# Kernel tuning notes

Hardware: AMD Instinct MI355X
Metric: run time of the kernel (lower is better)

The kernel has to match this reference:

```python
import jax, jax.numpy as jnp
import numpy as np

B, NX, NY = 4, 128, 128
DIM, DH, HEADS, LATENT, DOUT = 128, 64, 8, 64, 128
KM = 3
KD = DH * KM          # per-head low-rank-kernel dim (192)
SCALING = 1.0         # kernel_multiplier<=4 and softmax=False -> scaling_factor
ROT_SCALE = 64.0      # 1/min_freq of continuous RotaryEmbedding (min_freq=1/64)
EPS = 1e-5


def layer_norm(x, g, b):
    m = x.mean(-1, keepdims=True)
    v = jnp.var(x, axis=-1, keepdims=True)
    return (x - m) * jax.lax.rsqrt(v + EPS) * g + b


def pooling_reducer(x, Win, g, b, W1, b1, W2, b2):
    # x: [b, n, m, c] -> mean over axis 2 -> PreNorm(MLP with gated GELU) -> [b, n, latent]
    h = (x @ Win).mean(axis=2)
    h = layer_norm(h, g, b)
    h = h @ W1 + b1
    c = h.shape[-1] // 2
    h = jax.nn.gelu(h[..., :c], approximate=False) * h[..., c:]
    return h @ W2 + b2


def rotary(t, pos):
    # t: [b,h,n,d], pos: [n] continuous coordinates
    d = t.shape[-1]
    inv_freq = 1.0 / (10000.0 ** (jnp.arange(0, d, 2, dtype=jnp.float32) / d))
    f = (pos * ROT_SCALE)[:, None] * inv_freq          # [n, d//2]
    f = jnp.concatenate([f, f], axis=-1)               # [n, d]
    cos, sin = jnp.cos(f), jnp.sin(f)
    x1, x2 = jnp.split(t, 2, axis=-1)
    rot = jnp.concatenate([-x2, x1], axis=-1)          # rotate_half (half-split variant)
    return t * cos + rot * sin


def low_rank_kernel(u, pos, Wqk):
    # u: [b, n, latent] -> kernel K: [b, h, n, n]
    b, n, _ = u.shape
    qk = u @ Wqk                                       # [b, n, 2*h*KD]
    q, k = jnp.split(qk, 2, axis=-1)
    q = q.reshape(b, n, HEADS, KD).transpose(0, 2, 1, 3)
    k = k.reshape(b, n, HEADS, KD).transpose(0, 2, 1, 3)
    q = rotary(q, pos)
    k = rotary(k, pos)
    return jnp.einsum('bhid,bhjd->bhij', q, k) * SCALING


def setup_inputs():
    key = jax.random.key(0)
    ks = jax.random.split(key, 16)
    s = 0.02
    def rn(k, shape):
        return jax.random.normal(k, shape, dtype=jnp.float32) * s
    return {
        'u': jax.random.normal(ks[0], (B, NX, NY, DIM), dtype=jnp.float32),
        'pos_x': jnp.sort(jax.random.uniform(ks[1], (NX,), dtype=jnp.float32)),
        'pos_y': jnp.sort(jax.random.uniform(ks[2], (NY,), dtype=jnp.float32)),
        'ln_g': jnp.ones((DIM,), jnp.float32),
        'ln_b': jnp.zeros((DIM,), jnp.float32),
        'Wv': rn(ks[3], (DIM, HEADS * DH)),
        'Win': rn(ks[4], (DIM, DIM)),
        'px_Win': rn(ks[5], (DIM, DIM)),
        'px_g': jnp.ones((DIM,), jnp.float32),
        'px_b': jnp.zeros((DIM,), jnp.float32),
        'px_W1': rn(ks[6], (DIM, 2 * DIM)),
        'px_b1': jnp.zeros((2 * DIM,), jnp.float32),
        'px_W2': rn(ks[7], (DIM, LATENT)),
        'px_b2': jnp.zeros((LATENT,), jnp.float32),
        'py_Win': rn(ks[8], (DIM, DIM)),
        'py_g': jnp.ones((DIM,), jnp.float32),
        'py_b': jnp.zeros((DIM,), jnp.float32),
        'py_W1': rn(ks[9], (DIM, 2 * DIM)),
        'py_b1': jnp.zeros((2 * DIM,), jnp.float32),
        'py_W2': rn(ks[10], (DIM, LATENT)),
        'py_b2': jnp.zeros((LATENT,), jnp.float32),
        'Wqk_x': rn(ks[11], (LATENT, 2 * HEADS * KD)),
        'Wqk_y': rn(ks[12], (LATENT, 2 * HEADS * KD)),
        'Wo1': rn(ks[13], (HEADS * DH, DOUT)),
        'Wo2': rn(ks[14], (DOUT, DOUT)),
    }


def reference(u, pos_x, pos_y, ln_g, ln_b, Wv, Win,
              px_Win, px_g, px_b, px_W1, px_b1, px_W2, px_b2,
              py_Win, py_g, py_b, py_W1, py_b1, py_W2, py_b2,
              Wqk_x, Wqk_y, Wo1, Wo2):
    un = layer_norm(u, ln_g, ln_b)                      # [b,nx,ny,dim]
    v = un @ Wv                                         # [b,nx,ny,h*dh]
    ui = un @ Win
    ux = pooling_reducer(ui, px_Win, px_g, px_b, px_W1, px_b1, px_W2, px_b2)                       # [b,nx,L]
    uy = pooling_reducer(ui.transpose(0, 2, 1, 3), py_Win, py_g, py_b, py_W1, py_b1, py_W2, py_b2)  # [b,ny,L]
    kx = low_rank_kernel(ux, pos_x, Wqk_x)              # [b,h,nx,nx]
    ky = low_rank_kernel(uy, pos_y, Wqk_y)              # [b,h,ny,ny]
    b, nx, ny, _ = u.shape
    vphi = v.reshape(b, nx, ny, HEADS, DH).transpose(0, 3, 1, 2, 4)   # b h i l c
    t = jnp.einsum('bhij,bhjmc->bhimc', kx, vphi)       # attend along x axis
    t = jnp.einsum('bhlm,bhimc->bhilc', ky, t)          # attend along y axis
    t = t.transpose(0, 2, 3, 1, 4).reshape(b, nx, ny, HEADS * DH)
    # InstanceNorm2d applied to a channels-LAST tensor (as in the original repo):
    # torch treats dim1 (nx) as channels, normalizing over (ny, h*dh) per (b, nx), no affine.
    m = t.mean(axis=(2, 3), keepdims=True)
    var = t.var(axis=(2, 3), keepdims=True)
    t = (t - m) * jax.lax.rsqrt(var + EPS)
    h = jax.nn.gelu(t @ Wo1, approximate=False)
    return h @ Wo2
```

## Files before the change

kernel.cpp:

```cpp
#include <hip/hip_runtime.h>
#include <math.h>

#define ROWS 65536
#define KDD 192

typedef __attribute__((ext_vector_type(8))) short bfrag;
typedef __attribute__((ext_vector_type(4))) float facc;

__device__ inline unsigned short bf16r(float x) {
  union { float f; unsigned u; } v; v.f = x;
  unsigned r = v.u + 0x7fffu + ((v.u >> 16) & 1u);
  return (unsigned short)(r >> 16);
}
__device__ inline float bf2f(unsigned short h) {
  union { unsigned u; float f; } v; v.u = ((unsigned)h) << 16; return v.f;
}
__device__ inline float gelu_f(float x) {
  return x * 0.5f * (1.f + erff(x * 0.70710678f));
}
__device__ __forceinline__ void gload16(const void* g, void* l) {
  __builtin_amdgcn_global_load_lds((const __attribute__((address_space(1))) unsigned int*)g,
                                   (__attribute__((address_space(3))) unsigned int*)l,
                                   16, 0, 0);
}

__global__ __launch_bounds__(128) void k_ln(const float* __restrict__ x,
                                            const float* __restrict__ g,
                                            const float* __restrict__ bb,
                                            unsigned short* __restrict__ y) {
  int row = blockIdx.x;
  int t = threadIdx.x;
  float v = x[(size_t)row * 128 + t];
  float s = v, s2 = v * v;
  for (int off = 32; off > 0; off >>= 1) {
    s += __shfl_down(s, off, 64);
    s2 += __shfl_down(s2, off, 64);
  }
  __shared__ float ps[2], ps2[2];
  int wid = t >> 6, lane = t & 63;
  if (lane == 0) { ps[wid] = s; ps2[wid] = s2; }
  __syncthreads();
  float S = ps[0] + ps[1], S2 = ps2[0] + ps2[1];
  float mean = S * (1.f / 128.f);
  float var = S2 * (1.f / 128.f) - mean * mean;
  float r = rsqrtf(var + 1e-5f);
  y[(size_t)row * 128 + t] = bf16r((v - mean) * r * g[t] + bb[t]);
}

__global__ __launch_bounds__(128) void k_means(const unsigned short* __restrict__ un,
                                               float* __restrict__ mx, float* __restrict__ my) {
  int blk = blockIdx.x;
  int c = threadIdx.x;
  if (blk < 512) {
    const unsigned short* p = un + (size_t)blk * 16384 + c;
    float s = 0;
    for (int j = 0; j < 128; j++) s += bf2f(p[(size_t)j * 128]);
    mx[(size_t)blk * 128 + c] = s * (1.f / 128.f);
  } else {
    int bj = blk - 512;
    int b = bj >> 7, j = bj & 127;
    const unsigned short* p = un + (size_t)b * 2097152 + (size_t)j * 128 + c;
    float s = 0;
    for (int i = 0; i < 128; i++) s += bf2f(p[(size_t)i * 16384]);
    my[(size_t)bj * 128 + c] = s * (1.f / 128.f);
  }
}

__global__ __launch_bounds__(256) void k_wprep(const float* __restrict__ Wv,
                                               const float* __restrict__ Wo1,
                                               const float* __restrict__ Wo2,
                                               unsigned short* __restrict__ WvT,
                                               unsigned short* __restrict__ Wo1T,
                                               unsigned short* __restrict__ Wo2T,
                                               float* __restrict__ scol) {
  int blk = blockIdx.x, t = threadIdx.x;
  if (blk < 256) {
    int idx = blk * 256 + t;
    int c = idx >> 7, r = idx & 127;
    WvT[(size_t)c * 128 + r] = bf16r(Wv[(size_t)r * 512 + c]);
  } else if (blk < 512) {
    int idx = (blk - 256) * 256 + t;
    int n = idx >> 9, k = idx & 511;
    Wo1T[(size_t)n * 512 + k] = bf16r(Wo1[(size_t)k * 128 + n]);
  } else if (blk < 576) {
    int idx = (blk - 512) * 256 + t;
    int n = idx >> 7, k = idx & 127;
    Wo2T[n * 128 + k] = bf16r(Wo2[k * 128 + n]);
  } else {
    if (t < 128) {
      float a = 0;
      for (int k = 0; k < 512; k++) a += bf2f(bf16r(Wo1[k * 128 + t]));
      scol[t] = a;
    }
  }
}

__global__ __launch_bounds__(256) void k_gemmz(const float* __restrict__ A0,
                                               const float* __restrict__ B0,
                                               float* __restrict__ C0,
                                               const float* __restrict__ A1,
                                               const float* __restrict__ B1,
                                               float* __restrict__ C1,
                                               int K, int lda, int ldb, int ldc) {
  const float* A = blockIdx.z ? A1 : A0;
  const float* Bm = blockIdx.z ? B1 : B0;
  float* C = blockIdx.z ? C1 : C0;
  __shared__ float As[16][64];
  __shared__ float Bs[16][64];
  int tid = threadIdx.x;
  int n0 = blockIdx.x * 64, m0 = blockIdx.y * 64;
  int tx = tid & 15, ty = tid >> 4;
  float acc[4][4] = {};
  int la_m = tid >> 2, la_k = (tid & 3) * 4;
  int lb_k = tid >> 4, lb_n = (tid & 15) * 4;
  for (int k0 = 0; k0 < K; k0 += 16) {
    float4 a4 = *(const float4*)(A + (size_t)(m0 + la_m) * lda + k0 + la_k);
    As[la_k + 0][la_m] = a4.x; As[la_k + 1][la_m] = a4.y;
    As[la_k + 2][la_m] = a4.z; As[la_k + 3][la_m] = a4.w;
    float4 b4 = *(const float4*)(Bm + (size_t)(k0 + lb_k) * ldb + n0 + lb_n);
    *(float4*)&Bs[lb_k][lb_n] = b4;
    __syncthreads();
#pragma unroll
    for (int kk = 0; kk < 16; kk++) {
      float4 av = *(const float4*)&As[kk][ty * 4];
      float4 bv = *(const float4*)&Bs[kk][tx * 4];
      float a[4] = {av.x, av.y, av.z, av.w};
      float b[4] = {bv.x, bv.y, bv.z, bv.w};
#pragma unroll
      for (int i = 0; i < 4; i++)
#pragma unroll
        for (int j = 0; j < 4; j++) acc[i][j] += a[i] * b[j];
    }
    __syncthreads();
  }
#pragma unroll
  for (int i = 0; i < 4; i++) {
    float4 o;
    o.x = acc[i][0]; o.y = acc[i][1]; o.z = acc[i][2]; o.w = acc[i][3];
    *(float4*)(C + (size_t)(m0 + ty * 4 + i) * ldc + n0 + tx * 4) = o;
  }
}

__global__ __launch_bounds__(128) void k_pool2(const float* __restrict__ in0, const float* __restrict__ in1,
                                               const float* __restrict__ Wc0, const float* __restrict__ Wc1,
                                               const float* __restrict__ g0, const float* __restrict__ g1,
                                               const float* __restrict__ bb0, const float* __restrict__ bb1,
                                               const float* __restrict__ W10, const float* __restrict__ W11,
                                               const float* __restrict__ b10, const float* __restrict__ b11,
                                               const float* __restrict__ W20, const float* __restrict__ W21,
                                               const float* __restrict__ b20, const float* __restrict__ b21,
                                               float* __restrict__ o0, float* __restrict__ o1) {
  int sel = blockIdx.y;
  const float* in = sel ? in1 : in0;  const float* Wc = sel ? Wc1 : Wc0;
  const float* g = sel ? g1 : g0;     const float* bb = sel ? bb1 : bb0;
  const float* W1 = sel ? W11 : W10;  const float* b1 = sel ? b11 : b10;
  const float* W2 = sel ? W21 : W20;  const float* b2 = sel ? b21 : b20;
  float* out = sel ? o1 : o0;
  int row = blockIdx.x;
  int t = threadIdx.x;
  __shared__ float xin[128], h1[128], h3[128];
  __shared__ float ps[2], ps2[2];
  xin[t] = in[(size_t)row * 128 + t];
  __syncthreads();
  float a = 0;
  for (int k = 0; k < 128; k++) a += xin[k] * Wc[k * 128 + t];
  float s = a, s2 = a * a;
  for (int off = 32; off > 0; off >>= 1) {
    s += __shfl_down(s, off, 64);
    s2 += __shfl_down(s2, off, 64);
  }
  if ((t & 63) == 0) { ps[t >> 6] = s; ps2[t >> 6] = s2; }
  __syncthreads();
  float S = ps[0] + ps[1], S2 = ps2[0] + ps2[1];
  float mean = S * (1.f / 128.f);
  float var = S2 * (1.f / 128.f) - mean * mean;
  float r = rsqrtf(var + 1e-5f);
  h1[t] = (a - mean) * r * g[t] + bb[t];
  __syncthreads();
  float u1 = b1[t], u2 = b1[t + 128];
  for (int k = 0; k < 128; k++) {
    float hv = h1[k];
    u1 += hv * W1[k * 256 + t];
    u2 += hv * W1[k * 256 + t + 128];
  }
  h3[t] = gelu_f(u1) * u2;
  __syncthreads();
  if (t < 64) {
    float o = b2[t];
    for (int k = 0; k < 128; k++) o += h3[k] * W2[k * 64 + t];
    out[(size_t)row * 64 + t] = o;
  }
}

__global__ __launch_bounds__(192) void k_rot2(const float* __restrict__ qk0, const float* __restrict__ qk1,
                                              const float* __restrict__ pos0, const float* __restrict__ pos1,
                                              float* __restrict__ qr0, float* __restrict__ qr1,
                                              float* __restrict__ kr0, float* __restrict__ kr1) {
  int sel = blockIdx.y;
  const float* qk = sel ? qk1 : qk0;
  const float* pos = sel ? pos1 : pos0;
  float* qr = sel ? qr1 : qr0;
  float* kr = sel ? kr1 : kr0;
  int bn = blockIdx.x;
  int b = bn >> 7, n = bn & 127;
  int d = threadIdx.x;
  int fi = d % 96;
  float inv = expf(-logf(10000.f) * ((float)fi / 96.f));
  float f = pos[n] * 64.f * inv;
  float cs = cosf(f), sn = sinf(f);
  int partner = d < 96 ? d + 96 : d - 96;
  float sgn = d < 96 ? -1.f : 1.f;
  for (int h = 0; h < 8; h++) {
    float q = qk[(size_t)bn * 3072 + h * 192 + d];
    float qp = qk[(size_t)bn * 3072 + h * 192 + partner];
    float kx = qk[(size_t)bn * 3072 + 1536 + h * 192 + d];
    float kp = qk[(size_t)bn * 3072 + 1536 + h * 192 + partner];
    size_t o = ((size_t)(b * 8 + h) * 128 + n) * 192 + d;
    qr[o] = q * cs + sgn * qp * sn;
    kr[o] = kx * cs + sgn * kp * sn;
  }
}

__global__ __launch_bounds__(256) void k_qkt2(const float* __restrict__ Q0, const float* __restrict__ K0,
                                              unsigned short* __restrict__ C0,
                                              const float* __restrict__ Q1, const float* __restrict__ K1,
                                              unsigned short* __restrict__ C1) {
  int z = blockIdx.z;
  int bh = z & 31;
  const float* Qb = (z < 32 ? Q0 : Q1) + (size_t)bh * 128 * KDD;
  const float* Kb = (z < 32 ? K0 : K1) + (size_t)bh * 128 * KDD;
  unsigned short* Cb = (z < 32 ? C0 : C1) + (size_t)bh * 128 * 128;
  __shared__ float As[16][64];
  __shared__ float Bs[16][64];
  int tid = threadIdx.x;
  int i0 = blockIdx.y * 64, j0 = blockIdx.x * 64;
  int tx = tid & 15, ty = tid >> 4;
  float acc[4][4] = {};
  int l_m = tid >> 2, l_k = (tid & 3) * 4;
  for (int k0 = 0; k0 < KDD; k0 += 16) {
    float4 a4 = *(const float4*)(Qb + (size_t)(i0 + l_m) * KDD + k0 + l_k);
    As[l_k + 0][l_m] = a4.x; As[l_k + 1][l_m] = a4.y;
    As[l_k + 2][l_m] = a4.z; As[l_k + 3][l_m] = a4.w;
    float4 b4 = *(const float4*)(Kb + (size_t)(j0 + l_m) * KDD + k0 + l_k);
    Bs[l_k + 0][l_m] = b4.x; Bs[l_k + 1][l_m] = b4.y;
    Bs[l_k + 2][l_m] = b4.z; Bs[l_k + 3][l_m] = b4.w;
    __syncthreads();
#pragma unroll
    for (int kk = 0; kk < 16; kk++) {
      float4 av = *(const float4*)&As[kk][ty * 4];
      float4 bv = *(const float4*)&Bs[kk][tx * 4];
      float a[4] = {av.x, av.y, av.z, av.w};
      float b[4] = {bv.x, bv.y, bv.z, bv.w};
#pragma unroll
      for (int i = 0; i < 4; i++)
#pragma unroll
        for (int j = 0; j < 4; j++) acc[i][j] += a[i] * b[j];
    }
    __syncthreads();
  }
#pragma unroll
  for (int i = 0; i < 4; i++) {
    unsigned h0 = bf16r(acc[i][0]), h1 = bf16r(acc[i][1]);
    unsigned h2 = bf16r(acc[i][2]), h3 = bf16r(acc[i][3]);
    uint2 pk;
    pk.x = h0 | (h1 << 16);
    pk.y = h2 | (h3 << 16);
    *(uint2*)(Cb + (size_t)(i0 + ty * 4 + i) * 128 + j0 + tx * 4) = pk;
  }
}


__global__ __launch_bounds__(256) void k_vt(const unsigned short* __restrict__ WvT,
                                            const unsigned short* __restrict__ un,
                                            unsigned short* __restrict__ vT) {
  int nt = blockIdx.x;
  int mt = blockIdx.y;
  __shared__ __align__(16) unsigned short As[16384];
  __shared__ __align__(16) unsigned short Bs[16384];
  int tid = threadIdx.x;
  int w = tid >> 6, lane = tid & 63, quad = lane >> 4, l16 = lane & 15;
  {
    int r = tid >> 1, half = tid & 1;
    const unsigned short* sa = WvT + (size_t)(mt * 128 + r) * 128 + half * 64;
    const unsigned short* sbp = un + (size_t)(nt * 128 + r) * 128 + half * 64;
#pragma unroll
    for (int q = 0; q < 8; q++) {
      int c8 = half * 8 + q;
      int ph = ((c8 ^ (r & 15)) << 3);
      *(uint4*)&As[r * 128 + ph] = *(const uint4*)(sa + q * 8);
      *(uint4*)&Bs[r * 128 + ph] = *(const uint4*)(sbp + q * 8);
    }
  }
  __syncthreads();
  facc zf = {0.f, 0.f, 0.f, 0.f};
  facc acc[2][8];
#pragma unroll
  for (int a = 0; a < 2; a++)
#pragma unroll
    for (int bq = 0; bq < 8; bq++) acc[a][bq] = zf;
#pragma unroll
  for (int k0 = 0; k0 < 4; k0++) {
    bfrag av[2];
#pragma unroll
    for (int it = 0; it < 2; it++) {
      int row = (w + it * 4) * 16 + l16;
      av[it] = *(const bfrag*)&As[row * 128 + ((((k0 * 4 + quad) ^ l16)) << 3)];
    }
#pragma unroll
    for (int nt8 = 0; nt8 < 8; nt8++) {
      int row = nt8 * 16 + l16;
      bfrag bv = *(const bfrag*)&Bs[row * 128 + ((((k0 * 4 + quad) ^ l16)) << 3)];
      acc[0][nt8] = __builtin_amdgcn_mfma_f32_16x16x32_bf16(av[0], bv, acc[0][nt8], 0, 0, 0);
      acc[1][nt8] = __builtin_amdgcn_mfma_f32_16x16x32_bf16(av[1], bv, acc[1][nt8], 0, 0, 0);
    }
  }
  __syncthreads();
#pragma unroll
  for (int it = 0; it < 2; it++)
#pragma unroll
    for (int nt8 = 0; nt8 < 8; nt8++)
#pragma unroll
      for (int rr = 0; rr < 4; rr++) {
        int row = (w + it * 4) * 16 + quad * 4 + rr;
        int col = nt8 * 16 + l16;
        As[row * 128 + ((((col >> 3) ^ (row & 15)) << 3)) + (col & 7)] = bf16r(acc[it][nt8][rr]);
      }
  __syncthreads();
  {
    int r = tid >> 1, half = tid & 1;
    unsigned short* dst = vT + (size_t)(mt * 128 + r) * 65536 + (size_t)nt * 128 + half * 64;
#pragma unroll
    for (int q = 0; q < 8; q++) {
      int c8 = half * 8 + q;
      *(uint4*)(dst + q * 8) = *(const uint4*)&As[r * 128 + ((c8 ^ (r & 15)) << 3)];
    }
  }
}

__global__ __launch_bounds__(256, 2) void k_fuse12(const unsigned short* __restrict__ kxall,
                                                   const unsigned short* __restrict__ kyall,
                                                   const unsigned short* __restrict__ vT,
                                                   unsigned short* __restrict__ ttp,
                                                   float* __restrict__ sb,
                                                   float* __restrict__ s2b) {
  int blk = blockIdx.x;
  int bh = blk >> 4, strip = blk & 15;
  int b = bh >> 3, h = bh & 7;
  __shared__ __align__(16) unsigned short Ky[16384];
  __shared__ __align__(16) unsigned short Vs[16384];
  int tid = threadIdx.x;
  int w = tid >> 6, lane = tid & 63, quad = lane >> 4, l16 = lane & 15;
  int wr = w >> 1, wc = w & 1;

  {
    const unsigned short* kb = kyall + (size_t)bh * 16384;
#pragma unroll
    for (int q = 0; q < 8; q++) {
      int rbase = w * 32 + q * 4;
      int r = rbase + quad;
      gload16(kb + (size_t)r * 128 + ((l16 ^ (r & 15)) << 3), &Ky[rbase * 128]);
    }
  }
  bfrag axf[4][4];
  {
    const unsigned short* xb = kxall + (size_t)bh * 16384;
#pragma unroll
    for (int it = 0; it < 4; it++) {
      int i = (wr * 4 + it) * 16 + l16;
#pragma unroll
      for (int k0 = 0; k0 < 4; k0++)
        axf[it][k0] = *(const bfrag*)(xb + (size_t)i * 128 + k0 * 32 + quad * 8);
    }
  }

  float s[4] = {0.f, 0.f, 0.f, 0.f}, s2[4] = {0.f, 0.f, 0.f, 0.f};
  facc zf = {0.f, 0.f, 0.f, 0.f};

  for (int cc = 0; cc < 4; cc++) {
    int c = strip * 4 + cc;
    if (cc) __syncthreads();
    {
      const unsigned short* vb = vT + (size_t)(h * 64 + c) * 65536 + (size_t)b * 16384;
#pragma unroll
      for (int q = 0; q < 8; q++) {
        int rbase = w * 32 + q * 4;
        int r = rbase + quad;
        gload16(vb + (size_t)r * 128 + ((l16 ^ (r & 15)) << 3), &Vs[rbase * 128]);
      }
    }
    __syncthreads();

    facc a1[4][4];
#pragma unroll
    for (int xt = 0; xt < 4; xt++)
#pragma unroll
      for (int lt = 0; lt < 4; lt++) a1[xt][lt] = zf;
#pragma unroll
    for (int k0 = 0; k0 < 4; k0++) {
      int chunk = ((k0 * 4 + quad) ^ l16) << 3;
      bfrag av[4], bv[4];
#pragma unroll
      for (int xt = 0; xt < 4; xt++)
        av[xt] = *(const bfrag*)&Vs[((wr * 4 + xt) * 16 + l16) * 128 + chunk];
#pragma unroll
      for (int lt = 0; lt < 4; lt++)
        bv[lt] = *(const bfrag*)&Ky[((wc * 4 + lt) * 16 + l16) * 128 + chunk];
      __builtin_amdgcn_s_setprio(1);
#pragma unroll
      for (int xt = 0; xt < 4; xt++)
#pragma unroll
        for (int lt = 0; lt < 4; lt++)
          a1[xt][lt] = __builtin_amdgcn_mfma_f32_16x16x32_bf16(av[xt], bv[lt], a1[xt][lt], 0, 0, 0);
      __builtin_amdgcn_s_setprio(0);
    }
    __syncthreads();
#pragma unroll
    for (int xt = 0; xt < 4; xt++) {
      int xc = (wr * 4 + xt) * 2 + (quad >> 1);
      int xo = (quad & 1) * 4;
#pragma unroll
      for (int lt = 0; lt < 4; lt++) {
        int l = (wc * 4 + lt) * 16 + l16;
        unsigned p0 = (unsigned)bf16r(a1[xt][lt][0]) | ((unsigned)bf16r(a1[xt][lt][1]) << 16);
        unsigned p1 = (unsigned)bf16r(a1[xt][lt][2]) | ((unsigned)bf16r(a1[xt][lt][3]) << 16);
        uint2 p; p.x = p0; p.y = p1;
        *(uint2*)&Vs[l * 128 + ((xc ^ (l & 15)) << 3) + xo] = p;
      }
    }
    __syncthreads();

    facc a2[4][4];
#pragma unroll
    for (int st = 0; st < 4; st++)
#pragma unroll
      for (int it = 0; it < 4; it++) a2[st][it] = zf;
#pragma unroll
    for (int k0 = 0; k0 < 4; k0++) {
      int chunk = ((k0 * 4 + quad) ^ l16) << 3;
      bfrag sv[4];
#pragma unroll
      for (int st = 0; st < 4; st++)
        sv[st] = *(const bfrag*)&Vs[((wc * 4 + st) * 16 + l16) * 128 + chunk];
      __builtin_amdgcn_s_setprio(1);
#pragma unroll
      for (int st = 0; st < 4; st++)
#pragma unroll
        for (int it = 0; it < 4; it++)
          a2[st][it] = __builtin_amdgcn_mfma_f32_16x16x32_bf16(sv[st], axf[it][k0], a2[st][it], 0, 0, 0);
      __builtin_amdgcn_s_setprio(0);
    }
    {
      unsigned short* dst = ttp + ((size_t)(bh * 64 + c) << 14);
#pragma unroll
      for (int st = 0; st < 4; st++) {
        int l0 = (wc * 4 + st) * 16 + quad * 4;
#pragma unroll
        for (int it = 0; it < 4; it++) {
          int i = (wr * 4 + it) * 16 + l16;
          float f0 = a2[st][it][0], f1 = a2[st][it][1];
          float f2 = a2[st][it][2], f3 = a2[st][it][3];
          unsigned p0 = (unsigned)bf16r(f0) | ((unsigned)bf16r(f1) << 16);
          unsigned p1 = (unsigned)bf16r(f2) | ((unsigned)bf16r(f3) << 16);
          uint2 p; p.x = p0; p.y = p1;
          *(uint2*)(dst + (size_t)i * 128 + l0) = p;
          s[it] += (f0 + f1) + (f2 + f3);
          s2[it] += f0 * f0 + f1 * f1 + f2 * f2 + f3 * f3;
        }
      }
    }
  }
#pragma unroll
  for (int it = 0; it < 4; it++) {
    float v = s[it], v2 = s2[it];
    v += __shfl_xor(v, 16, 64);  v += __shfl_xor(v, 32, 64);
    v2 += __shfl_xor(v2, 16, 64); v2 += __shfl_xor(v2, 32, 64);
    if (quad == 0) {
      int i = (wr * 4 + it) * 16 + l16;
      atomicAdd(&sb[b * 128 + i], v);
      atomicAdd(&s2b[b * 128 + i], v2);
    }
  }
}

__global__ __launch_bounds__(256) void k_tail2(const unsigned short* __restrict__ ttp,
                                               const unsigned short* __restrict__ Wo1T,
                                               const unsigned short* __restrict__ Wo2T,
                                               float* __restrict__ out,
                                               const float* __restrict__ sb,
                                               const float* __restrict__ s2b,
                                               const float* __restrict__ sc) {
  int blk = blockIdx.x;
  int b = blk >> 7, i = blk & 127;
  __shared__ __align__(16) unsigned short As[16384];
  __shared__ __align__(16) unsigned short Bs[16384];
  int tid = threadIdx.x;
  int w = tid >> 6, lane = tid & 63, quad = lane >> 4, l16 = lane & 15;
  facc zf = {0.f, 0.f, 0.f, 0.f};
  facc a1[2][8];
#pragma unroll
  for (int a = 0; a < 2; a++)
#pragma unroll
    for (int bq = 0; bq < 8; bq++) a1[a][bq] = zf;
  for (int kc = 0; kc < 4; kc++) {
    if (kc) __syncthreads();
    {
      int r = tid >> 1, half = tid & 1;
      int hc = kc * 128 + r;
      const unsigned short* src = ttp + (((size_t)(b * 8 + (hc >> 6)) * 64 + (hc & 63)) * 128 + i) * 128 + half * 64;
#pragma unroll
      for (int q = 0; q < 8; q++) {
        uint4 v = *(const uint4*)(src + q * 8);
        unsigned short* pv = (unsigned short*)&v;
#pragma unroll
        for (int e = 0; e < 8; e++) {
          int l = half * 64 + q * 8 + e;
          As[l * 128 + (((r >> 3) ^ (l & 15)) << 3) + (r & 7)] = pv[e];
        }
      }
      const unsigned short* sB = Wo1T + (size_t)r * 512 + kc * 128 + half * 64;
#pragma unroll
      for (int q = 0; q < 8; q++) {
        int c8 = half * 8 + q;
        *(uint4*)&Bs[r * 128 + ((c8 ^ (r & 15)) << 3)] = *(const uint4*)(sB + q * 8);
      }
    }
    __syncthreads();
#pragma unroll
    for (int k0 = 0; k0 < 4; k0++) {
      bfrag av[2];
#pragma unroll
      for (int it = 0; it < 2; it++) {
        int row = (w + it * 4) * 16 + l16;
        av[it] = *(const bfrag*)&As[row * 128 + (((k0 * 4 + quad) ^ l16) << 3)];
      }
#pragma unroll
      for (int nt = 0; nt < 8; nt++) {
        int row = nt * 16 + l16;
        bfrag bv = *(const bfrag*)&Bs[row * 128 + (((k0 * 4 + quad) ^ l16) << 3)];
        a1[0][nt] = __builtin_amdgcn_mfma_f32_16x16x32_bf16(av[0], bv, a1[0][nt], 0, 0, 0);
        a1[1][nt] = __builtin_amdgcn_mfma_f32_16x16x32_bf16(av[1], bv, a1[1][nt], 0, 0, 0);
      }
    }
  }
  float S = sb[b * 128 + i], S2 = s2b[b * 128 + i];
  float mean = S * (1.f / 65536.f);
  float var = S2 * (1.f / 65536.f) - mean * mean;
  float rs = rsqrtf(var + 1e-5f);
  __syncthreads();
#pragma unroll
  for (int it = 0; it < 2; it++)
#pragma unroll
    for (int nt = 0; nt < 8; nt++) {
      int n1 = nt * 16 + l16;
      float scn = sc[n1];
#pragma unroll
      for (int rr = 0; rr < 4; rr++) {
        int l = (w + it * 4) * 16 + quad * 4 + rr;
        float val = (a1[it][nt][rr] - mean * scn) * rs;
        As[l * 128 + (((n1 >> 3) ^ (l & 15)) << 3) + (n1 & 7)] = bf16r(gelu_f(val));
      }
    }
  {
    int r = tid >> 1, half = tid & 1;
    const unsigned short* sB = Wo2T + (size_t)r * 128 + half * 64;
#pragma unroll
    for (int q = 0; q < 8; q++) {
      int c8 = half * 8 + q;
      *(uint4*)&Bs[r * 128 + ((c8 ^ (r & 15)) << 3)] = *(const uint4*)(sB + q * 8);
    }
  }
  __syncthreads();
  facc a2[2][8];
#pragma unroll
  for (int a = 0; a < 2; a++)
#pragma unroll
    for (int bq = 0; bq < 8; bq++) a2[a][bq] = zf;
#pragma unroll
  for (int k0 = 0; k0 < 4; k0++) {
    bfrag av[2];
#pragma unroll
    for (int it = 0; it < 2; it++) {
      int row = (w + it * 4) * 16 + l16;
      av[it] = *(const bfrag*)&As[row * 128 + (((k0 * 4 + quad) ^ l16) << 3)];
    }
#pragma unroll
    for (int nt = 0; nt < 8; nt++) {
      int row = nt * 16 + l16;
      bfrag bv = *(const bfrag*)&Bs[row * 128 + (((k0 * 4 + quad) ^ l16) << 3)];
      a2[0][nt] = __builtin_amdgcn_mfma_f32_16x16x32_bf16(av[0], bv, a2[0][nt], 0, 0, 0);
      a2[1][nt] = __builtin_amdgcn_mfma_f32_16x16x32_bf16(av[1], bv, a2[1][nt], 0, 0, 0);
    }
  }
#pragma unroll
  for (int it = 0; it < 2; it++)
#pragma unroll
    for (int nt = 0; nt < 8; nt++) {
      int n2 = nt * 16 + l16;
#pragma unroll
      for (int rr = 0; rr < 4; rr++) {
        int l = (w + it * 4) * 16 + quad * 4 + rr;
        out[((size_t)(b * 16384 + i * 128 + l)) * 128 + n2] = a2[it][nt][rr];
      }
    }
}

extern "C" void kernel_launch(void* const* d_in, const int* in_sizes, int n_in,
                              void* d_out, int out_size, void* d_ws, size_t ws_size,
                              hipStream_t stream) {
  const float* u = (const float*)d_in[0];
  const float* pos_x = (const float*)d_in[1];
  const float* pos_y = (const float*)d_in[2];
  const float* ln_g = (const float*)d_in[3];
  const float* ln_b = (const float*)d_in[4];
  const float* Wv = (const float*)d_in[5];
  const float* Win = (const float*)d_in[6];
  const float* px_Win = (const float*)d_in[7];
  const float* px_g = (const float*)d_in[8];
  const float* px_b = (const float*)d_in[9];
  const float* px_W1 = (const float*)d_in[10];
  const float* px_b1 = (const float*)d_in[11];
  const float* px_W2 = (const float*)d_in[12];
  const float* px_b2 = (const float*)d_in[13];
  const float* py_Win = (const float*)d_in[14];
  const float* py_g = (const float*)d_in[15];
  const float* py_b = (const float*)d_in[16];
  const float* py_W1 = (const float*)d_in[17];
  const float* py_b1 = (const float*)d_in[18];
  const float* py_W2 = (const float*)d_in[19];
  const float* py_b2 = (const float*)d_in[20];
  const float* Wqk_x = (const float*)d_in[21];
  const float* Wqk_y = (const float*)d_in[22];
  const float* Wo1 = (const float*)d_in[23];
  const float* Wo2 = (const float*)d_in[24];
  float* out = (float*)d_out;

  const size_t NEED = 44868736;
  if (ws_size < NEED * sizeof(float)) return;
  float* ws = (float*)d_ws;
  unsigned short* un_bf = (unsigned short*)ws;
  unsigned short* vT    = (unsigned short*)(ws + 4194304);
  unsigned short* ttp   = (unsigned short*)(ws + 20971520);
  float* small = ws + 37748736;
  float* mun_x = small;
  float* mun_y = small + 65536;
  float* Wcx   = small + 131072;
  float* Wcy   = small + 147456;
  float* ux    = small + 163840;
  float* uy    = small + 196608;
  float* qkx   = small + 229376;
  float* qky   = small + 1802240;
  float* qrx   = small + 3375104;
  float* krx   = small + 4161536;
  float* qry   = small + 4947968;
  float* kry   = small + 5734400;
  unsigned short* kx_bf = (unsigned short*)(small + 6520832);
  unsigned short* ky_bf = (unsigned short*)(small + 6782976);
  unsigned short* WvT   = (unsigned short*)(small + 7045120);
  unsigned short* Wo1T  = (unsigned short*)(small + 7077888);
  unsigned short* Wo2T  = (unsigned short*)(small + 7110656);
  float* sbuf  = small + 7118848;
  float* s2buf = small + 7119360;
  float* scol  = small + 7119872;

  hipMemsetAsync(sbuf, 0, 1024 * sizeof(float), stream);

  k_ln<<<ROWS, 128, 0, stream>>>(u, ln_g, ln_b, un_bf);
  k_means<<<1024, 128, 0, stream>>>(un_bf, mun_x, mun_y);
  k_wprep<<<577, 256, 0, stream>>>(Wv, Wo1, Wo2, WvT, Wo1T, Wo2T, scol);
  k_gemmz<<<dim3(2, 2, 2), 256, 0, stream>>>(Win, px_Win, Wcx, Win, py_Win, Wcy,
                                             128, 128, 128, 128);
  k_pool2<<<dim3(512, 2), 128, 0, stream>>>(mun_x, mun_y, Wcx, Wcy, px_g, py_g, px_b, py_b,
                                            px_W1, py_W1, px_b1, py_b1, px_W2, py_W2,
                                            px_b2, py_b2, ux, uy);
  k_gemmz<<<dim3(48, 8, 2), 256, 0, stream>>>(ux, Wqk_x, qkx, uy, Wqk_y, qky,
                                              64, 64, 3072, 3072);
  k_rot2<<<dim3(512, 2), 192, 0, stream>>>(qkx, qky, pos_x, pos_y, qrx, qry, krx, kry);
  k_qkt2<<<dim3(2, 2, 64), 256, 0, stream>>>(qrx, krx, kx_bf, qry, kry, ky_bf);

  k_vt<<<dim3(512, 4), 256, 0, stream>>>(WvT, un_bf, vT);
  k_fuse12<<<512, 256, 0, stream>>>(kx_bf, ky_bf, vT, ttp, sbuf, s2buf);
  k_tail2<<<512, 256, 0, stream>>>(ttp, Wo1T, Wo2T, out, sbuf, s2buf, scol);
}
```

Measured before the change: 337.2 us.

## Restructure V-projection kernel to reuse input tile across two weight tiles

Each block of the vT GEMM now loads its 128-row activation tile into LDS once, using direct global-to-LDS loads, and reuses it for two 128-column weight tiles, halving the grid. Weight fragments are read straight from global memory instead of being staged in LDS. The transposed bf16 output is written directly from registers, dropping the LDS round-trip and two barriers. In exchange the output stores are narrow strided 8-byte writes, and per-block work becomes more serial.

After: 326.3 us. 1.03x faster.

```diff
diff --git a/kernel.cpp b/kernel.cpp
--- a/kernel.cpp
+++ b/kernel.cpp
@@ -273,66 +273,63 @@
 __global__ __launch_bounds__(256) void k_vt(const unsigned short* __restrict__ WvT,
                                             const unsigned short* __restrict__ un,
                                             unsigned short* __restrict__ vT) {
-  int nt = blockIdx.x;
-  int mt = blockIdx.y;
-  __shared__ __align__(16) unsigned short As[16384];
+  int bx = blockIdx.x;
+  int nt = bx >> 1;
+  int mh = (bx & 1) * 2;
   __shared__ __align__(16) unsigned short Bs[16384];
   int tid = threadIdx.x;
   int w = tid >> 6, lane = tid & 63, quad = lane >> 4, l16 = lane & 15;
+  int wr = w >> 1, wc = w & 1;
   {
-    int r = tid >> 1, half = tid & 1;
-    const unsigned short* sa = WvT + (size_t)(mt * 128 + r) * 128 + half * 64;
-    const unsigned short* sbp = un + (size_t)(nt * 128 + r) * 128 + half * 64;
+    const unsigned short* sbp = un + (size_t)nt * 16384;
 #pragma unroll
     for (int q = 0; q < 8; q++) {
-      int c8 = half * 8 + q;
-      int ph = ((c8 ^ (r & 15)) << 3);
-      *(uint4*)&As[r * 128 + ph] = *(const uint4*)(sa + q * 8);
-      *(uint4*)&Bs[r * 128 + ph] = *(const uint4*)(sbp + q * 8);
+      int rbase = w * 32 + q * 4;
+      int r = rbase + quad;
+      gload16(sbp + (size_t)r * 128 + ((l16 ^ (r & 15)) << 3), &Bs[rbase * 128]);
     }
   }
   __syncthreads();
   facc zf = {0.f, 0.f, 0.f, 0.f};
-  facc acc[2][8];
-#pragma unroll
-  for (int a = 0; a < 2; a++)
-#pragma unroll
-    for (int bq = 0; bq < 8; bq++) acc[a][bq] = zf;
-#pragma unroll
-  for (int k0 = 0; k0 < 4; k0++) {
-    bfrag av[2];
-#pragma unroll
-    for (int it = 0; it < 2; it++) {
-      int row = (w + it * 4) * 16 + l16;
-      av[it] = *(const bfrag*)&As[row * 128 + ((((k0 * 4 + quad) ^ l16)) << 3)];
-    }
-#pragma unroll
-    for (int nt8 = 0; nt8 < 8; nt8++) {
-      int row = nt8 * 16 + l16;
-      bfrag bv = *(const bfrag*)&Bs[row * 128 + ((((k0 * 4 + quad) ^ l16)) << 3)];
-      acc[0][nt8] = __builtin_amdgcn_mfma_f32_16x16x32_bf16(av[0], bv, acc[0][nt8], 0, 0, 0);
-      acc[1][nt8] = __builtin_amdgcn_mfma_f32_16x16x32_bf16(av[1], bv, acc[1][nt8], 0, 0, 0);
-    }
-  }
-  __syncthreads();
-#pragma unroll
-  for (int it = 0; it < 2; it++)
-#pragma unroll
-    for (int nt8 = 0; nt8 < 8; nt8++)
-#pragma unroll
-      for (int rr = 0; rr < 4; rr++) {
-        int row = (w + it * 4) * 16 + quad * 4 + rr;
-        int col = nt8 * 16 + l16;
-        As[row * 128 + ((((col >> 3) ^ (row & 15)) << 3)) + (col & 7)] = bf16r(acc[it][nt8][rr]);
-      }
-  __syncthreads();
-  {
-    int r = tid >> 1, half = tid & 1;
-    unsigned short* dst = vT + (size_t)(mt * 128 + r) * 65536 + (size_t)nt * 128 + half * 64;
-#pragma unroll
-    for (int q = 0; q < 8; q++) {
-      int c8 = half * 8 + q;
-      *(uint4*)(dst + q * 8) = *(const uint4*)&As[r * 128 + ((c8 ^ (r & 15)) << 3)];
+#pragma unroll
+  for (int m2 = 0; m2 < 2; m2++) {
+    int mt = mh + m2;
+    const unsigned short* ap = WvT + (size_t)mt * 128 * 128;
+    facc acc[4][4];
+#pragma unroll
+    for (int lt = 0; lt < 4; lt++)
+#pragma unroll
+      for (int xt = 0; xt < 4; xt++) acc[lt][xt] = zf;
+#pragma unroll
+    for (int k0 = 0; k0 < 4; k0++) {
+      int chunk = ((k0 * 4 + quad) ^ l16) << 3;
+      bfrag bv[4], av[4];
+#pragma unroll
+      for (int lt = 0; lt < 4; lt++)
+        bv[lt] = *(const bfrag*)&Bs[((wc * 4 + lt) * 16 + l16) * 128 + chunk];
+#pragma unroll
+      for (int xt = 0; xt < 4; xt++)
+        av[xt] = *(const bfrag*)(ap + (size_t)((wr * 4 + xt) * 16 + l16) * 128 + k0 * 32 + quad * 8);
+      __builtin_amdgcn_s_setprio(1);
+#pragma unroll
+      for (int lt = 0; lt < 4; lt++)
+#pragma unroll
+        for (int xt = 0; xt < 4; xt++)
+          acc[lt][xt] = __builtin_amdgcn_mfma_f32_16x16x32_bf16(bv[lt], av[xt], acc[lt][xt], 0, 0, 0);
+      __builtin_amdgcn_s_setprio(0);
+    }
+#pragma unroll
+    for (int xt = 0; xt < 4; xt++) {
+      int hc = mt * 128 + (wr * 4 + xt) * 16 + l16;
+      unsigned short* dst = vT + (size_t)hc * 65536 + nt * 128 + quad * 4;
+#pragma unroll
+      for (int lt = 0; lt < 4; lt++) {
+        facc a = acc[lt][xt];
+        uint2 p;
+        p.x = (unsigned)bf16r(a[0]) | ((unsigned)bf16r(a[1]) << 16);
+        p.y = (unsigned)bf16r(a[2]) | ((unsigned)bf16r(a[3]) << 16);
+        *(uint2*)(dst + (wc * 4 + lt) * 16) = p;
+      }
     }
   }
 }
@@ -677,7 +674,7 @@
   k_rot2<<<dim3(512, 2), 192, 0, stream>>>(qkx, qky, pos_x, pos_y, qrx, qry, krx, kry);
   k_qkt2<<<dim3(2, 2, 64), 256, 0, stream>>>(qrx, krx, kx_bf, qry, kry, ky_bf);
 
-  k_vt<<<dim3(512, 4), 256, 0, stream>>>(WvT, un_bf, vT);
+  k_vt<<<1024, 256, 0, stream>>>(WvT, un_bf, vT);
   k_fuse12<<<512, 256, 0, stream>>>(kx_bf, ky_bf, vT, ttp, sbuf, s2buf);
   k_tail2<<<512, 256, 0, stream>>>(ttp, Wo1T, Wo2T, out, sbuf, s2buf, scol);
 }
```
